# Performance work log

Measured on AMD Instinct MI355X. Metric: run time of the kernel, lower is better.

The kernel has to match this reference:

```python
import jax, jax.numpy as jnp
import numpy as np

N_HEAD = 16

def setup_inputs() -> dict:
    key = jax.random.key(0)
    ks = jax.random.split(key, 5)
    B, T, C = 4, 2048, 1024
    s = 0.02
    return {
        "x": jax.random.normal(ks[0], (B, T, C), dtype=jnp.float32),
        "W_attn": jax.random.normal(ks[1], (C, 3 * C), dtype=jnp.float32) * s,
        "b_attn": jax.random.normal(ks[2], (3 * C,), dtype=jnp.float32) * s,
        "W_proj": jax.random.normal(ks[3], (C, C), dtype=jnp.float32) * s,
        "b_proj": jax.random.normal(ks[4], (C,), dtype=jnp.float32) * s,
    }

def reference(x, W_attn, b_attn, W_proj, b_proj):
    B, T, C = x.shape
    H = N_HEAD
    D = C // H
    qkv = x @ W_attn + b_attn                      # [B,T,3C]
    q, k, v = jnp.split(qkv, 3, axis=2)
    # [B,H,T,D]
    q = q.reshape(B, T, H, D).transpose(0, 2, 1, 3)
    k = k.reshape(B, T, H, D).transpose(0, 2, 1, 3)
    v = v.reshape(B, T, H, D).transpose(0, 2, 1, 3)
    scale = 1.0 / jnp.sqrt(jnp.float32(D))
    att = jnp.einsum('bhqd,bhkd->bhqk', q, k) * scale
    causal = jnp.tril(jnp.ones((T, T), dtype=bool))
    att = jnp.where(causal[None, None], att, -jnp.inf)
    att = jax.nn.softmax(att, axis=-1)
    y = jnp.einsum('bhqk,bhkd->bhqd', att, v)       # [B,H,T,D]
    y = y.transpose(0, 2, 1, 3).reshape(B, T, C)
    return y @ W_proj + b_proj
```

## Files before the change

### kernel.cpp

```cpp
#include <hip/hip_runtime.h>

typedef unsigned short u16;
typedef unsigned int u32;
typedef __bf16 bf16x8 __attribute__((ext_vector_type(8)));
typedef short s16x4 __attribute__((ext_vector_type(4)));
typedef float f32x4 __attribute__((ext_vector_type(4)));

#define MFMA16(a,b,c) __builtin_amdgcn_mfma_f32_16x16x32_bf16((a),(b),(c),0,0,0)

#if defined(__has_builtin)
#if __has_builtin(__builtin_amdgcn_mfma_f32_16x16x16bf16_1k)
#define MFMA1K(a,b,c) __builtin_amdgcn_mfma_f32_16x16x16bf16_1k((a),(b),(c),0,0,0)
#endif
#endif
#ifndef MFMA1K
__device__ __forceinline__ f32x4 mfma1k_asm(s16x4 a, s16x4 b, f32x4 c) {
    f32x4 d;
    asm volatile("v_mfma_f32_16x16x16_bf16 %0, %1, %2, %3"
                 : "=v"(d) : "v"(a), "v"(b), "0"(c));
    return d;
}
#define MFMA1K(a,b,c) mfma1k_asm((a),(b),(c))
#endif

__device__ __forceinline__ float b2f(u16 u) {
    u32 v = ((u32)u) << 16;
    return __builtin_bit_cast(float, v);
}
__device__ __forceinline__ u16 f2b(float f) {
    u32 u = __builtin_bit_cast(u32, f);
    u = u + 0x7FFFu + ((u >> 16) & 1u);
    return (u16)(u >> 16);
}

__device__ __forceinline__ void gload_lds16(const u16* g, u16* l) {
    __builtin_amdgcn_global_load_lds(
        (__attribute__((address_space(1))) void*)g,
        (__attribute__((address_space(3))) void*)l, 16, 0, 0);
}

__device__ __forceinline__ uint4 load8_bf16(const void* base, size_t off, int f32m) {
    if (f32m) {
        const float* p = (const float*)base + off;
        float4 a = *(const float4*)p;
        float4 b = *(const float4*)(p + 4);
        union { u16 u[8]; uint4 v; } t;
        t.u[0] = f2b(a.x); t.u[1] = f2b(a.y); t.u[2] = f2b(a.z); t.u[3] = f2b(a.w);
        t.u[4] = f2b(b.x); t.u[5] = f2b(b.y); t.u[6] = f2b(b.z); t.u[7] = f2b(b.w);
        return t.v;
    }
    return *(const uint4*)((const u16*)base + off);
}

__device__ __forceinline__ int detect_f32(const u16* __restrict__ x) {
    __shared__ int cnt;
    if (threadIdx.x == 0) cnt = 0;
    __syncthreads();
    int my = ((x[2 * (threadIdx.x * 128)] >> 7) & 0xFF) >= 0x90;
    unsigned long long b = __ballot(my);
    if ((threadIdx.x & 63) == 0) atomicAdd(&cnt, (int)__popcll(b));
    __syncthreads();
    return cnt > 32;
}

__device__ __forceinline__ void transpose_tile(
    const void* __restrict__ src, u16* __restrict__ dst, int R, int Cc,
    int f32m, int bx, int by)
{
    __shared__ u16 tile[64 * 72];
    const int t = threadIdx.x;
    const int c0 = bx * 64, r0 = by * 64;
    #pragma unroll
    for (int i = 0; i < 2; ++i) {
        int ch = t + 256 * i;
        int r = ch >> 3, c8 = (ch & 7) * 8;
        *(uint4*)&tile[r * 72 + c8] =
            load8_bf16(src, (size_t)(r0 + r) * Cc + c0 + c8, f32m);
    }
    __syncthreads();
    #pragma unroll
    for (int i = 0; i < 2; ++i) {
        int ch = t + 256 * i;
        int r = ch >> 3, c8 = (ch & 7) * 8;
        union { u16 u[8]; uint4 v; } tmp;
        #pragma unroll
        for (int j = 0; j < 8; ++j) tmp.u[j] = tile[(c8 + j) * 72 + r];
        *(uint4*)&dst[(size_t)(c0 + r) * R + r0 + c8] = tmp.v;
    }
}

__global__ __launch_bounds__(256) void k_prep(
    const u16* __restrict__ x, const void* __restrict__ Wa,
    const void* __restrict__ ba, const void* __restrict__ Wp,
    const void* __restrict__ bp,
    u16* __restrict__ WaT, u16* __restrict__ WpT, u16* __restrict__ Abf,
    u16* __restrict__ bac, u16* __restrict__ bpc, int* __restrict__ flag)
{
    const int f32m = detect_f32(x);
    int task = blockIdx.x;
    if (task < 768) {
        transpose_tile(Wa, WaT, 1024, 3072, f32m, task % 48, task / 48);
        return;
    }
    task -= 768;
    if (task < 256) {
        transpose_tile(Wp, WpT, 1024, 1024, f32m, task % 16, task / 16);
        return;
    }
    task -= 256;
    if (task < 4096) {
        if (!f32m) return;
        size_t i = ((size_t)task * 256 + threadIdx.x) * 8;
        const float* xf = (const float*)x;
        float4 a = *(const float4*)(xf + i);
        float4 b = *(const float4*)(xf + i + 4);
        union { u16 u[8]; uint4 v; } t;
        t.u[0] = f2b(a.x); t.u[1] = f2b(a.y); t.u[2] = f2b(a.z); t.u[3] = f2b(a.w);
        t.u[4] = f2b(b.x); t.u[5] = f2b(b.y); t.u[6] = f2b(b.z); t.u[7] = f2b(b.w);
        *(uint4*)(Abf + i) = t.v;
        return;
    }
    const int t = threadIdx.x;
    #pragma unroll
    for (int j = 0; j < 12; ++j) {
        int i = t + 256 * j;
        if (i < 3072) bac[i] = f32m ? f2b(((const float*)ba)[i]) : ((const u16*)ba)[i];
    }
    #pragma unroll
    for (int j = 0; j < 4; ++j) {
        int i = t + 256 * j;
        if (i < 1024) bpc[i] = f32m ? f2b(((const float*)bp)[i]) : ((const u16*)bp)[i];
    }
    if (t == 0) *flag = f32m;
}


__device__ __forceinline__ void stage8(const u16* __restrict__ Asrc,
                                       const u16* __restrict__ Bsrc,
                                       u16* Asb, u16* Bsb, int wbase, int lane)
{
    #pragma unroll
    for (int i = 0; i < 4; ++i) {
        int gbase = wbase + 512 * i;
        int g = gbase | lane;
        int r = g >> 3, u = (g & 7) ^ (r & 7);
        gload_lds16(Asrc + (size_t)r * 1024 + u * 8, Asb + gbase * 8);
    }
    #pragma unroll
    for (int i = 0; i < 4; ++i) {
        int gbase = wbase + 512 * i;
        int g = gbase | lane;
        int r = g >> 3, u = (g & 7) ^ (r & 7);
        gload_lds16(Bsrc + (size_t)r * 1024 + u * 8, Bsb + gbase * 8);
    }
}

__device__ __forceinline__ void stage6(const u16* __restrict__ Asrc,
                                       const u16* __restrict__ Bsrc,
                                       u16* Asb, u16* Bsb, int wbase, int lane)
{
    #pragma unroll
    for (int i = 0; i < 4; ++i) {
        int gbase = wbase + 512 * i;
        int g = gbase | lane;
        int gg = (g & ~7) | ((g & 7) ^ ((g >> 3) & 7));
        gload_lds16(Asrc + gg * 8, Asb + gbase * 8);
    }
    #pragma unroll
    for (int i = 0; i < 2; ++i) {
        int gbase = wbase + 512 * i;
        int g = gbase | lane;
        int r = g >> 3, u = (g & 7) ^ (r & 7);
        gload_lds16(Bsrc + (size_t)r * 1024 + u * 8, Bsb + gbase * 8);
    }
}

__device__ __forceinline__ const u16* frag_ptr(const u16* base, int R, int sl) {
    int gr = (R << 3) | (sl ^ (R & 7));
    return base + gr * 8;
}

__global__ __launch_bounds__(512, 2) void k_gemm_qkv(
    const void* __restrict__ x, const u16* __restrict__ Abf,
    const u16* __restrict__ Bt, const u16* __restrict__ bias,
    const int* __restrict__ flag,
    u16* __restrict__ Ql, u16* __restrict__ Kl, u16* __restrict__ Vl)
{
    __shared__ __align__(16) u16 As[2][16384];
    __shared__ __align__(16) u16 Bs[2][16384];
    const int t = threadIdx.x;
    const int lane = t & 63, w = t >> 6;
    const int wbase = t & ~63;
    const int quad = lane >> 4, m16 = lane & 15;
    const int wr = w >> 2, wc = w & 3;
    const int m0 = blockIdx.x * 256, n0 = blockIdx.y * 256;
    const u16* A = (*flag) ? Abf : (const u16*)x;

    const u16* Atile = A + (size_t)m0 * 1024;
    const u16* Btile = Bt + (size_t)n0 * 1024;

    const f32x4 z = {0.f, 0.f, 0.f, 0.f};
    f32x4 acc[8][4];
    #pragma unroll
    for (int mi = 0; mi < 8; ++mi)
        #pragma unroll
        for (int ni = 0; ni < 4; ++ni) acc[mi][ni] = z;

    stage8(Atile,      Btile,      &As[0][0], &Bs[0][0], wbase, lane);
    stage8(Atile + 64, Btile + 64, &As[1][0], &Bs[1][0], wbase, lane);
    __builtin_amdgcn_sched_barrier(0);
    asm volatile("s_waitcnt vmcnt(8)" ::: "memory");
    __builtin_amdgcn_s_barrier();
    __builtin_amdgcn_sched_barrier(0);

    for (int kt = 0; kt < 16; ++kt) {
        const u16* Asb = &As[kt & 1][0];
        const u16* Bsb = &Bs[kt & 1][0];

        bf16x8 bfr[4][2];
        #pragma unroll
        for (int ni = 0; ni < 4; ++ni)
            #pragma unroll
            for (int kk = 0; kk < 2; ++kk)
                bfr[ni][kk] = *(const bf16x8*)frag_ptr(Bsb, wc * 64 + ni * 16 + m16, kk * 4 + quad);

        #pragma unroll
        for (int ph = 0; ph < 4; ++ph) {
            bf16x8 af[2][2];
            #pragma unroll
            for (int m2 = 0; m2 < 2; ++m2)
                #pragma unroll
                for (int kk = 0; kk < 2; ++kk)
                    af[m2][kk] = *(const bf16x8*)frag_ptr(
                        Asb, wr * 128 + (ph * 2 + m2) * 16 + m16, kk * 4 + quad);
            __builtin_amdgcn_s_setprio(1);
            #pragma unroll
            for (int m2 = 0; m2 < 2; ++m2)
                #pragma unroll
                for (int ni = 0; ni < 4; ++ni) {
                    acc[ph * 2 + m2][ni] = MFMA16(af[m2][0], bfr[ni][0], acc[ph * 2 + m2][ni]);
                    acc[ph * 2 + m2][ni] = MFMA16(af[m2][1], bfr[ni][1], acc[ph * 2 + m2][ni]);
                }
            __builtin_amdgcn_s_setprio(0);
        }

        __builtin_amdgcn_sched_barrier(0);
        __builtin_amdgcn_s_barrier();
        if (kt < 14)
            stage8(Atile + (kt + 2) * 64, Btile + (kt + 2) * 64,
                   (u16*)Asb, (u16*)Bsb, wbase, lane);
        __builtin_amdgcn_sched_barrier(0);
        if (kt < 14) asm volatile("s_waitcnt vmcnt(8)" ::: "memory");
        else         asm volatile("s_waitcnt vmcnt(0)" ::: "memory");
        __builtin_amdgcn_s_barrier();
        __builtin_amdgcn_sched_barrier(0);
    }

    const int sec = n0 >> 10;
    const float qscale = (sec == 0) ? 0.18033688011112042f : 1.0f;
    u16* Outp = (sec == 0) ? Ql : (sec == 1) ? Kl : Vl;
    #pragma unroll
    for (int mi = 0; mi < 8; ++mi) {
        #pragma unroll
        for (int ni = 0; ni < 4; ++ni) {
            int gn = n0 + wc * 64 + ni * 16 + m16;
            int sn = gn & 1023;
            int h = sn >> 6, d = sn & 63;
            float bv = b2f(bias[gn]);
            #pragma unroll
            for (int v = 0; v < 4; ++v) {
                int gm = m0 + wr * 128 + mi * 16 + quad * 4 + v;
                int bb = gm >> 11, tt = gm & 2047;
                u16 o = f2b((acc[mi][ni][v] + bv) * qscale);
                size_t bh = (size_t)(bb * 16 + h);
                Outp[(bh * 2048 + tt) * 64 + d] = o;
            }
        }
    }
}

__global__ __launch_bounds__(256) void k_attn(
    u16* __restrict__ Ql, const u16* __restrict__ Kl, const u16* __restrict__ Vl)
{
    __shared__ u16 Ks[128 * 80];
    __shared__ u16 Vs[64 * 132];
    const int t = threadIdx.x;
    const int lane = t & 63, w = t >> 6;
    const int quad = lane >> 4, m16 = lane & 15;
    const int g = blockIdx.x >> 6;
    const int p = g >> 2, r = g & 3;
    const int qb = (p == 0) ? 15 - r : (p == 1) ? 8 + r : (p == 2) ? 7 - r : r;
    const int bh = blockIdx.x & 63;
    const int q0 = qb * 128;

    bf16x8 fq[2][2];
    #pragma unroll
    for (int s = 0; s < 2; ++s) {
        const u16* Qp = Ql + ((size_t)bh * 2048 + q0 + s * 64 + w * 16 + m16) * 64;
        fq[s][0] = *(const bf16x8*)&Qp[quad * 8];
        fq[s][1] = *(const bf16x8*)&Qp[32 + quad * 8];
    }

    const f32x4 z = {0.f, 0.f, 0.f, 0.f};
    f32x4 acco[2][4] = {{z, z, z, z}, {z, z, z, z}};
    f32x4 accl[2] = {z, z};
    s16x4 ones4;
    #pragma unroll
    for (int j = 0; j < 4; ++j) ones4[j] = (short)0x3F80;

    const int ktmax = qb;
    const u16* Kbase = Kl + (size_t)bh * 2048 * 64;
    const u16* Vbase = Vl + (size_t)bh * 2048 * 64;

    uint4 kreg[4], vreg[4];
    #pragma unroll
    for (int i = 0; i < 4; ++i) {
        int c = t + 256 * i;
        int rr = c >> 3, col = (c & 7) * 8;
        kreg[i] = *(const uint4*)&Kbase[(size_t)rr * 64 + col];
        vreg[i] = *(const uint4*)&Vbase[(size_t)rr * 64 + col];
    }

    for (int kt = 0; kt <= ktmax; ++kt) {
        __syncthreads();
        #pragma unroll
        for (int i = 0; i < 4; ++i) {
            int c = t + 256 * i;
            int rr = c >> 3, col = (c & 7) * 8;
            *(uint4*)&Ks[rr * 80 + col] = kreg[i];
            union { u16 u[8]; uint4 v; } tv; tv.v = vreg[i];
            #pragma unroll
            for (int j = 0; j < 8; ++j)
                Vs[(col + j) * 132 + rr] = tv.u[j];
        }
        __syncthreads();

        if (kt < ktmax) {
            #pragma unroll
            for (int i = 0; i < 4; ++i) {
                int c = t + 256 * i;
                int rr = c >> 3, col = (c & 7) * 8;
                kreg[i] = *(const uint4*)&Kbase[(size_t)((kt + 1) * 128 + rr) * 64 + col];
                vreg[i] = *(const uint4*)&Vbase[(size_t)((kt + 1) * 128 + rr) * 64 + col];
            }
        }

        const bool diag = (kt == ktmax);
        #pragma unroll
        for (int s = 0; s < 2; ++s) {
            f32x4 accs[8] = {z, z, z, z, z, z, z, z};
            __builtin_amdgcn_s_setprio(1);
            #pragma unroll
            for (int kk = 0; kk < 2; ++kk)
                #pragma unroll
                for (int ni = 0; ni < 8; ++ni) {
                    bf16x8 bk = *(const bf16x8*)&Ks[(ni * 16 + m16) * 80 + kk * 32 + quad * 8];
                    accs[ni] = MFMA16(bk, fq[s][kk], accs[ni]);
                }
            __builtin_amdgcn_s_setprio(0);

            s16x4 pkv[8];
            if (!diag) {
                #pragma unroll
                for (int ni = 0; ni < 8; ++ni) {
                    union { __bf16 b[4]; s16x4 sv; } pk;
                    #pragma unroll
                    for (int v = 0; v < 4; ++v)
                        pk.b[v] = (__bf16)__builtin_amdgcn_exp2f(accs[ni][v]);
                    pkv[ni] = pk.sv;
                }
            } else {
                const int qg = q0 + s * 64 + w * 16 + m16;
                #pragma unroll
                for (int ni = 0; ni < 8; ++ni) {
                    union { __bf16 b[4]; s16x4 sv; } pk;
                    #pragma unroll
                    for (int v = 0; v < 4; ++v) {
                        float sc = accs[ni][v];
                        if (kt * 128 + ni * 16 + quad * 4 + v > qg) sc = -30000.0f;
                        pk.b[v] = (__bf16)__builtin_amdgcn_exp2f(sc);
                    }
                    pkv[ni] = pk.sv;
                }
            }

            __builtin_amdgcn_s_setprio(1);
            #pragma unroll
            for (int ni = 0; ni < 8; ++ni) {
                #pragma unroll
                for (int nd = 0; nd < 4; ++nd) {
                    s16x4 va = *(const s16x4*)&Vs[(nd * 16 + m16) * 132 + ni * 16 + quad * 4];
                    acco[s][nd] = MFMA1K(va, pkv[ni], acco[s][nd]);
                }
                accl[s] = MFMA1K(ones4, pkv[ni], accl[s]);
            }
            __builtin_amdgcn_s_setprio(0);
        }
    }

    #pragma unroll
    for (int s = 0; s < 2; ++s) {
        const int qg = q0 + s * 64 + w * 16 + m16;
        const float inv = 1.0f / fmaxf(accl[s][0], 1e-30f);
        u16* Orow = &Ql[((size_t)bh * 2048 + qg) * 64];
        #pragma unroll
        for (int nd = 0; nd < 4; ++nd) {
            union { u16 u[4]; uint2 uu; } o;
            #pragma unroll
            for (int v = 0; v < 4; ++v) o.u[v] = f2b(acco[s][nd][v] * inv);
            *(uint2*)&Orow[nd * 16 + quad * 4] = o.uu;
        }
    }
}

__global__ __launch_bounds__(512, 2) void k_gemm_proj(
    const u16* __restrict__ Yl, const u16* __restrict__ Bt, const u16* __restrict__ bias,
    const int* __restrict__ flag, void* __restrict__ Out)
{
    __shared__ __align__(16) u16 As[2][16384];
    __shared__ __align__(16) u16 Bs[2][8192];
    const int f32m = *flag;
    const int t = threadIdx.x;
    const int lane = t & 63, w = t >> 6;
    const int wbase = t & ~63;
    const int quad = lane >> 4, m16 = lane & 15;
    const int wr = w >> 2, wc = w & 3;
    const int m0 = blockIdx.x * 256, n0 = blockIdx.y * 128;
    const int bb = m0 >> 11, t0 = m0 & 2047;

    const u16* Btile = Bt + (size_t)n0 * 1024;
    #define ABASE(KT) (Yl + ((size_t)(bb * 16 + (KT)) * 2048 + t0) * 64)

    const f32x4 z = {0.f, 0.f, 0.f, 0.f};
    f32x4 acc[8][2];
    #pragma unroll
    for (int mi = 0; mi < 8; ++mi)
        #pragma unroll
        for (int ni = 0; ni < 2; ++ni) acc[mi][ni] = z;

    stage6(ABASE(0), Btile,      &As[0][0], &Bs[0][0], wbase, lane);
    stage6(ABASE(1), Btile + 64, &As[1][0], &Bs[1][0], wbase, lane);
    __builtin_amdgcn_sched_barrier(0);
    asm volatile("s_waitcnt vmcnt(6)" ::: "memory");
    __builtin_amdgcn_s_barrier();
    __builtin_amdgcn_sched_barrier(0);

    for (int kt = 0; kt < 16; ++kt) {
        const u16* Asb = &As[kt & 1][0];
        const u16* Bsb = &Bs[kt & 1][0];

        bf16x8 bfr[2][2];
        #pragma unroll
        for (int ni = 0; ni < 2; ++ni)
            #pragma unroll
            for (int kk = 0; kk < 2; ++kk)
                bfr[ni][kk] = *(const bf16x8*)frag_ptr(Bsb, wc * 32 + ni * 16 + m16, kk * 4 + quad);

        #pragma unroll
        for (int ph = 0; ph < 4; ++ph) {
            bf16x8 af[2][2];
            #pragma unroll
            for (int m2 = 0; m2 < 2; ++m2)
                #pragma unroll
                for (int kk = 0; kk < 2; ++kk)
                    af[m2][kk] = *(const bf16x8*)frag_ptr(
                        Asb, wr * 128 + (ph * 2 + m2) * 16 + m16, kk * 4 + quad);
            __builtin_amdgcn_s_setprio(1);
            #pragma unroll
            for (int m2 = 0; m2 < 2; ++m2)
                #pragma unroll
                for (int ni = 0; ni < 2; ++ni) {
                    acc[ph * 2 + m2][ni] = MFMA16(af[m2][0], bfr[ni][0], acc[ph * 2 + m2][ni]);
                    acc[ph * 2 + m2][ni] = MFMA16(af[m2][1], bfr[ni][1], acc[ph * 2 + m2][ni]);
                }
            __builtin_amdgcn_s_setprio(0);
        }

        __builtin_amdgcn_sched_barrier(0);
        __builtin_amdgcn_s_barrier();
        if (kt < 14)
            stage6(ABASE(kt + 2), Btile + (kt + 2) * 64,
                   (u16*)Asb, (u16*)Bsb, wbase, lane);
        __builtin_amdgcn_sched_barrier(0);
        if (kt < 14) asm volatile("s_waitcnt vmcnt(6)" ::: "memory");
        else         asm volatile("s_waitcnt vmcnt(0)" ::: "memory");
        __builtin_amdgcn_s_barrier();
        __builtin_amdgcn_sched_barrier(0);
    }
    #undef ABASE

    #pragma unroll
    for (int mi = 0; mi < 8; ++mi) {
        #pragma unroll
        for (int ni = 0; ni < 2; ++ni) {
            int gn = n0 + wc * 32 + ni * 16 + m16;
            float bv = b2f(bias[gn]);
            #pragma unroll
            for (int v = 0; v < 4; ++v) {
                int gm = m0 + wr * 128 + mi * 16 + quad * 4 + v;
                float val = acc[mi][ni][v] + bv;
                if (f32m) ((float*)Out)[(size_t)gm * 1024 + gn] = val;
                else      ((u16*)Out)[(size_t)gm * 1024 + gn] = f2b(val);
            }
        }
    }
}

extern "C" void kernel_launch(void* const* d_in, const int* in_sizes, int n_in,
                              void* d_out, int out_size, void* d_ws, size_t ws_size,
                              hipStream_t stream)
{
    (void)in_sizes; (void)n_in; (void)out_size; (void)ws_size;
    const void* x  = d_in[0];
    const void* Wa = d_in[1];
    const void* ba = d_in[2];
    const void* Wp = d_in[3];
    const void* bp = d_in[4];
    char* ws = (char*)d_ws;

    u16* Ql  = (u16*)(ws + 0);
    u16* Kl  = (u16*)(ws + 16777216);
    u16* Vl  = (u16*)(ws + 33554432);
    u16* WpT = (u16*)(ws + 50331648);
    int* flag = (int*)(ws + 52428800);
    u16* bpc  = (u16*)(ws + 52428800 + 256);
    u16* bac  = (u16*)(ws + 52428800 + 256 + 2048);
    u16* WaT = (u16*)d_out;
    u16* Abf = (u16*)((char*)d_out + 6291456);

    k_prep<<<5121, 256, 0, stream>>>((const u16*)x, Wa, ba, Wp, bp,
                                     WaT, WpT, Abf, bac, bpc, flag);
    k_gemm_qkv<<<dim3(32, 12), 512, 0, stream>>>(x, Abf, WaT, bac, flag, Ql, Kl, Vl);
    k_attn<<<1024, 256, 0, stream>>>(Ql, Kl, Vl);
    k_gemm_proj<<<dim3(32, 8), 512, 0, stream>>>(Ql, WpT, bpc, flag, d_out);
}
```

Before: 276.8 us.

## Shrink QKV GEMM N-tile, swizzle attention K smem, interleave score/PV per key block

The QKV GEMM tile drops from 256x256 to 256x128, which doubles the grid to 768 blocks for better CU fill, and the two-blocks-per-CU launch bound is removed. In attention, K shared memory changes from a padded stride-80 layout to an XOR-swizzled stride-64 layout read through frag_ptr. The score, exp and PV loop is restructured per 16-key slice, handling both query halves together so B-operand loads are reused and fewer score registers stay live. The attention launch bound now requests 4 blocks per SM. The smaller GEMM tile lowers arithmetic intensity and adds A-operand reloads.

```diff
diff --git a/kernel.cpp b/kernel.cpp
--- a/kernel.cpp
+++ b/kernel.cpp
@@ -135,9 +135,9 @@
 }
 
 
-__device__ __forceinline__ void stage8(const u16* __restrict__ Asrc,
-                                       const u16* __restrict__ Bsrc,
-                                       u16* Asb, u16* Bsb, int wbase, int lane)
+__device__ __forceinline__ void stage_qkv(const u16* __restrict__ Asrc,
+                                          const u16* __restrict__ Bsrc,
+                                          u16* Asb, u16* Bsb, int wbase, int lane)
 {
     #pragma unroll
     for (int i = 0; i < 4; ++i) {
@@ -147,7 +147,7 @@
         gload_lds16(Asrc + (size_t)r * 1024 + u * 8, Asb + gbase * 8);
     }
     #pragma unroll
-    for (int i = 0; i < 4; ++i) {
+    for (int i = 0; i < 2; ++i) {
         int gbase = wbase + 512 * i;
         int g = gbase | lane;
         int r = g >> 3, u = (g & 7) ^ (r & 7);
@@ -180,36 +180,36 @@
     return base + gr * 8;
 }
 
-__global__ __launch_bounds__(512, 2) void k_gemm_qkv(
+__global__ __launch_bounds__(512) void k_gemm_qkv(
     const void* __restrict__ x, const u16* __restrict__ Abf,
     const u16* __restrict__ Bt, const u16* __restrict__ bias,
     const int* __restrict__ flag,
     u16* __restrict__ Ql, u16* __restrict__ Kl, u16* __restrict__ Vl)
 {
     __shared__ __align__(16) u16 As[2][16384];
-    __shared__ __align__(16) u16 Bs[2][16384];
+    __shared__ __align__(16) u16 Bs[2][8192];
     const int t = threadIdx.x;
     const int lane = t & 63, w = t >> 6;
     const int wbase = t & ~63;
     const int quad = lane >> 4, m16 = lane & 15;
     const int wr = w >> 2, wc = w & 3;
-    const int m0 = blockIdx.x * 256, n0 = blockIdx.y * 256;
+    const int m0 = blockIdx.x * 256, n0 = blockIdx.y * 128;
     const u16* A = (*flag) ? Abf : (const u16*)x;
 
     const u16* Atile = A + (size_t)m0 * 1024;
     const u16* Btile = Bt + (size_t)n0 * 1024;
 
     const f32x4 z = {0.f, 0.f, 0.f, 0.f};
-    f32x4 acc[8][4];
+    f32x4 acc[8][2];
     #pragma unroll
     for (int mi = 0; mi < 8; ++mi)
         #pragma unroll
-        for (int ni = 0; ni < 4; ++ni) acc[mi][ni] = z;
-
-    stage8(Atile,      Btile,      &As[0][0], &Bs[0][0], wbase, lane);
-    stage8(Atile + 64, Btile + 64, &As[1][0], &Bs[1][0], wbase, lane);
+        for (int ni = 0; ni < 2; ++ni) acc[mi][ni] = z;
+
+    stage_qkv(Atile,      Btile,      &As[0][0], &Bs[0][0], wbase, lane);
+    stage_qkv(Atile + 64, Btile + 64, &As[1][0], &Bs[1][0], wbase, lane);
     __builtin_amdgcn_sched_barrier(0);
-    asm volatile("s_waitcnt vmcnt(8)" ::: "memory");
+    asm volatile("s_waitcnt vmcnt(6)" ::: "memory");
     __builtin_amdgcn_s_barrier();
     __builtin_amdgcn_sched_barrier(0);
 
@@ -217,12 +217,12 @@
         const u16* Asb = &As[kt & 1][0];
         const u16* Bsb = &Bs[kt & 1][0];
 
-        bf16x8 bfr[4][2];
-        #pragma unroll
-        for (int ni = 0; ni < 4; ++ni)
+        bf16x8 bfr[2][2];
+        #pragma unroll
+        for (int ni = 0; ni < 2; ++ni)
             #pragma unroll
             for (int kk = 0; kk < 2; ++kk)
-                bfr[ni][kk] = *(const bf16x8*)frag_ptr(Bsb, wc * 64 + ni * 16 + m16, kk * 4 + quad);
+                bfr[ni][kk] = *(const bf16x8*)frag_ptr(Bsb, wc * 32 + ni * 16 + m16, kk * 4 + quad);
 
         #pragma unroll
         for (int ph = 0; ph < 4; ++ph) {
@@ -237,7 +237,7 @@
             #pragma unroll
             for (int m2 = 0; m2 < 2; ++m2)
                 #pragma unroll
-                for (int ni = 0; ni < 4; ++ni) {
+                for (int ni = 0; ni < 2; ++ni) {
                     acc[ph * 2 + m2][ni] = MFMA16(af[m2][0], bfr[ni][0], acc[ph * 2 + m2][ni]);
                     acc[ph * 2 + m2][ni] = MFMA16(af[m2][1], bfr[ni][1], acc[ph * 2 + m2][ni]);
                 }
@@ -247,10 +247,10 @@
         __builtin_amdgcn_sched_barrier(0);
         __builtin_amdgcn_s_barrier();
         if (kt < 14)
-            stage8(Atile + (kt + 2) * 64, Btile + (kt + 2) * 64,
-                   (u16*)Asb, (u16*)Bsb, wbase, lane);
+            stage_qkv(Atile + (kt + 2) * 64, Btile + (kt + 2) * 64,
+                      (u16*)Asb, (u16*)Bsb, wbase, lane);
         __builtin_amdgcn_sched_barrier(0);
-        if (kt < 14) asm volatile("s_waitcnt vmcnt(8)" ::: "memory");
+        if (kt < 14) asm volatile("s_waitcnt vmcnt(6)" ::: "memory");
         else         asm volatile("s_waitcnt vmcnt(0)" ::: "memory");
         __builtin_amdgcn_s_barrier();
         __builtin_amdgcn_sched_barrier(0);
@@ -262,8 +262,8 @@
     #pragma unroll
     for (int mi = 0; mi < 8; ++mi) {
         #pragma unroll
-        for (int ni = 0; ni < 4; ++ni) {
-            int gn = n0 + wc * 64 + ni * 16 + m16;
+        for (int ni = 0; ni < 2; ++ni) {
+            int gn = n0 + wc * 32 + ni * 16 + m16;
             int sn = gn & 1023;
             int h = sn >> 6, d = sn & 63;
             float bv = b2f(bias[gn]);
@@ -279,10 +279,10 @@
     }
 }
 
-__global__ __launch_bounds__(256) void k_attn(
+__global__ __launch_bounds__(256, 4) void k_attn(
     u16* __restrict__ Ql, const u16* __restrict__ Kl, const u16* __restrict__ Vl)
 {
-    __shared__ u16 Ks[128 * 80];
+    __shared__ __align__(16) u16 Ks[128 * 64];
     __shared__ u16 Vs[64 * 132];
     const int t = threadIdx.x;
     const int lane = t & 63, w = t >> 6;
@@ -316,8 +316,10 @@
     #pragma unroll
     for (int i = 0; i < 4; ++i) {
         int c = t + 256 * i;
-        int rr = c >> 3, col = (c & 7) * 8;
-        kreg[i] = *(const uint4*)&Kbase[(size_t)rr * 64 + col];
+        int rr = c >> 3;
+        int ucol = ((c & 7) ^ (rr & 7)) * 8;
+        int col = (c & 7) * 8;
+        kreg[i] = *(const uint4*)&Kbase[(size_t)rr * 64 + ucol];
         vreg[i] = *(const uint4*)&Vbase[(size_t)rr * 64 + col];
     }
 
@@ -327,7 +329,7 @@
         for (int i = 0; i < 4; ++i) {
             int c = t + 256 * i;
             int rr = c >> 3, col = (c & 7) * 8;
-            *(uint4*)&Ks[rr * 80 + col] = kreg[i];
+            *(uint4*)&Ks[c * 8] = kreg[i];
             union { u16 u[8]; uint4 v; } tv; tv.v = vreg[i];
             #pragma unroll
             for (int j = 0; j < 8; ++j)
@@ -339,61 +341,60 @@
             #pragma unroll
             for (int i = 0; i < 4; ++i) {
                 int c = t + 256 * i;
-                int rr = c >> 3, col = (c & 7) * 8;
-                kreg[i] = *(const uint4*)&Kbase[(size_t)((kt + 1) * 128 + rr) * 64 + col];
+                int rr = c >> 3;
+                int ucol = ((c & 7) ^ (rr & 7)) * 8;
+                int col = (c & 7) * 8;
+                kreg[i] = *(const uint4*)&Kbase[(size_t)((kt + 1) * 128 + rr) * 64 + ucol];
                 vreg[i] = *(const uint4*)&Vbase[(size_t)((kt + 1) * 128 + rr) * 64 + col];
             }
         }
 
         const bool diag = (kt == ktmax);
-        #pragma unroll
-        for (int s = 0; s < 2; ++s) {
-            f32x4 accs[8] = {z, z, z, z, z, z, z, z};
+        const int qg0 = q0 + w * 16 + m16;
+        #pragma unroll
+        for (int ni = 0; ni < 8; ++ni) {
+            const int R = ni * 16 + m16;
+            bf16x8 bk0 = *(const bf16x8*)frag_ptr(Ks, R, quad);
+            bf16x8 bk1 = *(const bf16x8*)frag_ptr(Ks, R, 4 + quad);
+            f32x4 as0 = z, as1 = z;
             __builtin_amdgcn_s_setprio(1);
-            #pragma unroll
-            for (int kk = 0; kk < 2; ++kk)
-                #pragma unroll
-                for (int ni = 0; ni < 8; ++ni) {
-                    bf16x8 bk = *(const bf16x8*)&Ks[(ni * 16 + m16) * 80 + kk * 32 + quad * 8];
-                    accs[ni] = MFMA16(bk, fq[s][kk], accs[ni]);
-                }
+            as0 = MFMA16(bk0, fq[0][0], as0);
+            as1 = MFMA16(bk0, fq[1][0], as1);
+            as0 = MFMA16(bk1, fq[0][1], as0);
+            as1 = MFMA16(bk1, fq[1][1], as1);
             __builtin_amdgcn_s_setprio(0);
 
-            s16x4 pkv[8];
-            if (!diag) {
-                #pragma unroll
-                for (int ni = 0; ni < 8; ++ni) {
-                    union { __bf16 b[4]; s16x4 sv; } pk;
-                    #pragma unroll
-                    for (int v = 0; v < 4; ++v)
-                        pk.b[v] = (__bf16)__builtin_amdgcn_exp2f(accs[ni][v]);
-                    pkv[ni] = pk.sv;
-                }
-            } else {
-                const int qg = q0 + s * 64 + w * 16 + m16;
-                #pragma unroll
-                for (int ni = 0; ni < 8; ++ni) {
-                    union { __bf16 b[4]; s16x4 sv; } pk;
+            s16x4 p0, p1;
+            {
+                union { __bf16 b[4]; s16x4 sv; } pa, pb;
+                if (!diag) {
                     #pragma unroll
                     for (int v = 0; v < 4; ++v) {
-                        float sc = accs[ni][v];
-                        if (kt * 128 + ni * 16 + quad * 4 + v > qg) sc = -30000.0f;
-                        pk.b[v] = (__bf16)__builtin_amdgcn_exp2f(sc);
+                        pa.b[v] = (__bf16)__builtin_amdgcn_exp2f(as0[v]);
+                        pb.b[v] = (__bf16)__builtin_amdgcn_exp2f(as1[v]);
                     }
-                    pkv[ni] = pk.sv;
+                } else {
+                    #pragma unroll
+                    for (int v = 0; v < 4; ++v) {
+                        int kv = kt * 128 + ni * 16 + quad * 4 + v;
+                        float s0 = (kv > qg0)      ? -30000.0f : as0[v];
+                        float s1 = (kv > qg0 + 64) ? -30000.0f : as1[v];
+                        pa.b[v] = (__bf16)__builtin_amdgcn_exp2f(s0);
+                        pb.b[v] = (__bf16)__builtin_amdgcn_exp2f(s1);
+                    }
                 }
+                p0 = pa.sv; p1 = pb.sv;
             }
 
             __builtin_amdgcn_s_setprio(1);
             #pragma unroll
-            for (int ni = 0; ni < 8; ++ni) {
-                #pragma unroll
-                for (int nd = 0; nd < 4; ++nd) {
-                    s16x4 va = *(const s16x4*)&Vs[(nd * 16 + m16) * 132 + ni * 16 + quad * 4];
-                    acco[s][nd] = MFMA1K(va, pkv[ni], acco[s][nd]);
-                }
-                accl[s] = MFMA1K(ones4, pkv[ni], accl[s]);
+            for (int nd = 0; nd < 4; ++nd) {
+                s16x4 va = *(const s16x4*)&Vs[(nd * 16 + m16) * 132 + ni * 16 + quad * 4];
+                acco[0][nd] = MFMA1K(va, p0, acco[0][nd]);
+                acco[1][nd] = MFMA1K(va, p1, acco[1][nd]);
             }
+            accl[0] = MFMA1K(ones4, p0, accl[0]);
+            accl[1] = MFMA1K(ones4, p1, accl[1]);
             __builtin_amdgcn_s_setprio(0);
         }
     }
@@ -530,7 +531,7 @@
 
     k_prep<<<5121, 256, 0, stream>>>((const u16*)x, Wa, ba, Wp, bp,
                                      WaT, WpT, Abf, bac, bpc, flag);
-    k_gemm_qkv<<<dim3(32, 12), 512, 0, stream>>>(x, Abf, WaT, bac, flag, Ql, Kl, Vl);
+    k_gemm_qkv<<<dim3(32, 24), 512, 0, stream>>>(x, Abf, WaT, bac, flag, Ql, Kl, Vl);
     k_attn<<<1024, 256, 0, stream>>>(Ql, Kl, Vl);
     k_gemm_proj<<<dim3(32, 8), 512, 0, stream>>>(Ql, WpT, bpc, flag, d_out);
 }
```

Measured after the change: 309.4 us. 1.12x slower.
